# Kernel optimization log

Measured on AMD Instinct MI355X. Metric: run time of the kernel, lower is better.

The kernel has to match this reference:

```python
import jax, jax.numpy as jnp
import numpy as np

NUM_LABELS = 80
GROUPS = 512
OUT_PER_GROUP = 4  # 2048 / 512
K = 14  # kernel == spatial size -> 1x1 output


def setup_inputs() -> dict:
    key = jax.random.key(0)
    ks = jax.random.split(key, 8)
    B = 256
    x = jax.random.normal(ks[0], (B, NUM_LABELS, K, K), dtype=jnp.float32)
    # conv1: 1x1, num_labels -> 512 (store as [out,in])
    w1 = jax.random.normal(ks[1], (512, NUM_LABELS), dtype=jnp.float32) * 0.05
    b1 = jax.random.normal(ks[2], (512,), dtype=jnp.float32) * 0.01
    # conv2: 1x1, 512 -> 512
    w2 = jax.random.normal(ks[3], (512, 512), dtype=jnp.float32) * 0.05
    b2 = jax.random.normal(ks[4], (512,), dtype=jnp.float32) * 0.01
    # conv3 (grouped): per group, 1 in-ch -> 4 out-ch, 14x14 kernel, no bias
    w3 = jax.random.normal(ks[5], (GROUPS, OUT_PER_GROUP, K, K), dtype=jnp.float32) * 0.02
    # fc: 2048 -> num_labels (torch Linear layout [out,in])
    fc_w = jax.random.normal(ks[6], (NUM_LABELS, GROUPS * OUT_PER_GROUP), dtype=jnp.float32) * 0.02
    fc_b = jax.random.normal(ks[7], (NUM_LABELS,), dtype=jnp.float32) * 0.01
    return {"x": x, "w1": w1, "b1": b1, "w2": w2, "b2": b2,
            "w3": w3, "fc_w": fc_w, "fc_b": fc_b}


def reference(x, w1, b1, w2, b2, w3, fc_w, fc_b):
    # conv1: 1x1 conv == channel GEMM. x: [B,C,H,W]
    h = jnp.einsum('bchw,oc->bohw', x, w1) + b1[None, :, None, None]
    # conv2: 1x1 conv, 512 -> 512
    h = jnp.einsum('bchw,oc->bohw', h, w2) + b2[None, :, None, None]
    # conv3: 512 independent group convs (1 in-ch each, full 14x14 kernel,
    # no padding) -> output spatial 1x1. Fused into a single contraction.
    # h: [B, G, H, W], w3: [G, O, H, W] -> [B, G, O]
    g = jnp.einsum('bghw,gohw->bgo', h, w3)
    g = jax.nn.relu(g)
    # torch.cat over groups then flatten == reshape [B, G*O]
    flat = g.reshape(g.shape[0], GROUPS * OUT_PER_GROUP)
    return flat @ fc_w.T + fc_b
```

## Files before the change

### kernel.cpp

```cpp
#include <hip/hip_runtime.h>
#include <hip/hip_bf16.h>

#define CIN 80
#define NSP 196
#define HWP 208
#define KP  96
#define XST 104

#define NBA 4096
#define NBB 1024
#define NBC 512
#define NBD 64
#define NBE 16

typedef __attribute__((ext_vector_type(8))) short  short8;
typedef __attribute__((ext_vector_type(4))) float  floatx4;
typedef __attribute__((ext_vector_type(4))) unsigned short ushort4v;

static __device__ __forceinline__ unsigned short f2b(float f) {
    __hip_bfloat16 h = __float2bfloat16(f);
    return *(unsigned short*)&h;
}
static __device__ __forceinline__ float b2f(unsigned short u) {
    unsigned int x = ((unsigned int)u) << 16;
    float f; __builtin_memcpy(&f, &x, 4); return f;
}

__global__ __launch_bounds__(384) void kPre(
    const float* __restrict__ x,  const float* __restrict__ w1,
    const float* __restrict__ b1, const float* __restrict__ w2,
    const float* __restrict__ b2, const float* __restrict__ w3,
    const float* __restrict__ fc_w, const float* __restrict__ fc_b,
    float* __restrict__ Wcf, unsigned short* __restrict__ xbf,
    unsigned short* __restrict__ w3tb, unsigned short* __restrict__ fctb,
    float* __restrict__ out)
{
    __shared__ float tile[80 * 53];
    const int blk = blockIdx.x, t = threadIdx.x;

    if (blk < NBA) {
        const int o4 = blk >> 5, kc = blk & 31;
        const int lc = t % 96, oi = t / 96;
        const int o = o4 * 4 + oi;
        const int m0 = kc * 16;
        if (lc <= CIN) {
            const float* __restrict__ w2p = w2 + (size_t)o * 512 + m0;
            float part = 0.f;
            if (lc < CIN) {
                const float* __restrict__ w1p = w1 + (size_t)m0 * CIN + lc;
                #pragma unroll
                for (int i = 0; i < 16; ++i)
                    part = fmaf(w2p[i], w1p[(size_t)i * CIN], part);
            } else {
                #pragma unroll
                for (int i = 0; i < 16; ++i)
                    part = fmaf(w2p[i], b1[m0 + i], part);
                if (kc == 31) part += b2[o];
            }
            atomicAdd(Wcf + o * KP + lc, part);
        }
    } else if (blk < NBA + NBB) {
        const int r = blk - NBA;
        const int b = r >> 2, qt = r & 3, hw0 = qt * 52;
        for (int idx = t; idx < 80 * 52; idx += 384) {
            const int k = idx / 52, hl = idx - k * 52;
            const int hw = hw0 + hl;
            tile[k * 53 + hl] = (hw < NSP) ? x[(size_t)b * CIN * NSP + k * NSP + hw] : 0.f;
        }
        __syncthreads();
        unsigned short* __restrict__ ob = xbf + (size_t)b * HWP * KP;
        for (int idx = t; idx < 52 * 24; idx += 384) {
            const int hl = idx / 24, kq = idx - hl * 24;
            const int hw = hw0 + hl;
            ushort4v v;
            #pragma unroll
            for (int j = 0; j < 4; ++j) {
                const int k = kq * 4 + j;
                float f = 0.f;
                if (hw < NSP) {
                    if (k < CIN) f = tile[k * 53 + hl];
                    else if (k == CIN) f = 1.f;
                }
                v[j] = f2b(f);
            }
            *(ushort4v*)(ob + (size_t)hw * KP + kq * 4) = v;
        }
    } else if (blk < NBA + NBB + NBC) {
        const int g = blk - NBA - NBB;
        if (t < HWP) {
            ushort4v v;
            #pragma unroll
            for (int o = 0; o < 4; ++o)
                v[o] = f2b((t < NSP) ? w3[(size_t)g * 4 * NSP + o * NSP + t] : 0.f);
            *(ushort4v*)(w3tb + ((size_t)g * HWP + t) * 4) = v;
        }
    } else if (blk < NBA + NBB + NBC + NBD) {
        const int base = (blk - NBA - NBB - NBC) * 2560;
        for (int i = t; i < 2560; i += 384) {
            const int idx = base + i;
            const int k = idx / CIN, l = idx - k * CIN;
            fctb[idx] = f2b(fc_w[(size_t)l * 2048 + k]);
        }
    } else {
        const int base = (blk - NBA - NBB - NBC - NBD) * 1280;
        for (int i = t; i < 1280; i += 384) {
            const int idx = base + i;
            out[idx] = fc_b[idx - (idx / CIN) * CIN];
        }
    }
}

__global__ __launch_bounds__(512) void kM(
    const unsigned short* __restrict__ xbf, const float* __restrict__ Wcf,
    const unsigned short* __restrict__ w3tb, const unsigned short* __restrict__ fctb,
    float* __restrict__ out)
{
    __shared__ __align__(16) unsigned short xs[HWP * XST];
    __shared__ float gl[512];
    const int b = blockIdx.x, gc = blockIdx.y;
    const int t = threadIdx.x;

    {
        const ushort4v* __restrict__ src = (const ushort4v*)(xbf + (size_t)b * HWP * KP);
        for (int idx = t; idx < HWP * 24; idx += 512) {
            const int r = idx / 24, c = idx - r * 24;
            *(ushort4v*)(xs + r * XST + c * 4) = src[r * 24 + c];
        }
    }

    const int w = t >> 6, lane = t & 63;
    const int col = lane & 15, quad = lane >> 4;
    const int g0 = gc * 128 + w * 16;

    short8 A[3];
    {
        const float* __restrict__ ap = Wcf + (size_t)(g0 + col) * KP + quad * 8;
        #pragma unroll
        for (int ks = 0; ks < 3; ++ks) {
            const floatx4 lo = *(const floatx4*)(ap + ks * 32);
            const floatx4 hi = *(const floatx4*)(ap + ks * 32 + 4);
            short8 s;
            #pragma unroll
            for (int j = 0; j < 4; ++j) {
                s[j]     = (short)f2b(lo[j]);
                s[4 + j] = (short)f2b(hi[j]);
            }
            A[ks] = s;
        }
    }

    float p[4][4];
    #pragma unroll
    for (int r = 0; r < 4; ++r)
        #pragma unroll
        for (int o = 0; o < 4; ++o) p[r][o] = 0.f;

    const unsigned short* __restrict__ wb =
        w3tb + ((size_t)(g0 + quad * 4) * HWP + col) * 4;
    const unsigned short* __restrict__ xrow = xs + col * XST + quad * 8;

    __syncthreads();

    ushort4v cw[4];
    #pragma unroll
    for (int r = 0; r < 4; ++r)
        cw[r] = *(const ushort4v*)(wb + (size_t)r * HWP * 4);

    #pragma unroll 1
    for (int nt = 0; nt < 13; ++nt) {
        const int ntn = (nt < 12) ? nt + 1 : 12;
        ushort4v nw[4];
        #pragma unroll
        for (int r = 0; r < 4; ++r)
            nw[r] = *(const ushort4v*)(wb + ((size_t)r * HWP + ntn * 16) * 4);

        const unsigned short* __restrict__ xp = xrow + nt * 16 * XST;
        const short8 x0 = *(const short8*)(xp);
        const short8 x1 = *(const short8*)(xp + 32);
        const short8 x2 = *(const short8*)(xp + 64);
        floatx4 acc = {0.f, 0.f, 0.f, 0.f};
        acc = __builtin_amdgcn_mfma_f32_16x16x32_bf16(A[0], x0, acc, 0, 0, 0);
        acc = __builtin_amdgcn_mfma_f32_16x16x32_bf16(A[1], x1, acc, 0, 0, 0);
        acc = __builtin_amdgcn_mfma_f32_16x16x32_bf16(A[2], x2, acc, 0, 0, 0);

        #pragma unroll
        for (int r = 0; r < 4; ++r) {
            p[r][0] = fmaf(acc[r], b2f(cw[r][0]), p[r][0]);
            p[r][1] = fmaf(acc[r], b2f(cw[r][1]), p[r][1]);
            p[r][2] = fmaf(acc[r], b2f(cw[r][2]), p[r][2]);
            p[r][3] = fmaf(acc[r], b2f(cw[r][3]), p[r][3]);
        }
        #pragma unroll
        for (int r = 0; r < 4; ++r) cw[r] = nw[r];
    }

    #pragma unroll
    for (int r = 0; r < 4; ++r) {
        float q0 = p[r][0], q1 = p[r][1], q2 = p[r][2], q3 = p[r][3];
        #pragma unroll
        for (int s = 8; s >= 1; s >>= 1) {
            q0 += __shfl_down(q0, s, 16);
            q1 += __shfl_down(q1, s, 16);
            q2 += __shfl_down(q2, s, 16);
            q3 += __shfl_down(q3, s, 16);
        }
        if (col == 0) {
            const int glocal = w * 16 + quad * 4 + r;
            floatx4 ov = {fmaxf(q0, 0.f), fmaxf(q1, 0.f), fmaxf(q2, 0.f), fmaxf(q3, 0.f)};
            *(floatx4*)(gl + glocal * 4) = ov;
        }
    }
    __syncthreads();

    if (t < 320) {
        const int l = t % CIN, q = t / CIN;
        const unsigned short* __restrict__ fr =
            fctb + (size_t)(gc * 512 + q * 128) * CIN + l;
        const float* __restrict__ gp = gl + q * 128;
        float s = 0.f;
        #pragma unroll 4
        for (int kk = 0; kk < 128; ++kk)
            s = fmaf(gp[kk], b2f(fr[(size_t)kk * CIN]), s);
        atomicAdd(out + b * CIN + l, s);
    }
}

extern "C" void kernel_launch(void* const* d_in, const int* in_sizes, int n_in,
                              void* d_out, int out_size, void* d_ws, size_t ws_size,
                              hipStream_t stream) {
    const float* x    = (const float*)d_in[0];
    const float* w1   = (const float*)d_in[1];
    const float* b1   = (const float*)d_in[2];
    const float* w2   = (const float*)d_in[3];
    const float* b2   = (const float*)d_in[4];
    const float* w3   = (const float*)d_in[5];
    const float* fc_w = (const float*)d_in[6];
    const float* fc_b = (const float*)d_in[7];
    float* out = (float*)d_out;

    const int B = in_sizes[0] / (CIN * NSP);

    char* ws = (char*)d_ws;
    unsigned short* xbf = (unsigned short*)ws;
    size_t off = (size_t)B * HWP * KP * 2;
    float* Wcf = (float*)(ws + off);                   off += 512 * KP * 4;
    unsigned short* w3tb = (unsigned short*)(ws + off); off += (size_t)512 * HWP * 4 * 2;
    unsigned short* fctb = (unsigned short*)(ws + off);

    hipMemsetAsync(Wcf, 0, 512 * KP * 4, stream);
    kPre<<<NBA + NBB + NBC + NBD + NBE, 384, 0, stream>>>(
        x, w1, b1, w2, b2, w3, fc_w, fc_b, Wcf, xbf, w3tb, fctb, out);
    kM<<<dim3(B, 4), 512, 0, stream>>>(xbf, Wcf, w3tb, fctb, out);
}
```

Baseline: 139.4 us.

## Process two M-tiles per warp and halve grid to reuse staged x tile

Each block now covers 256 groups instead of 128, with each warp computing two 16-row MFMA tiles that share the same x fragments from shared memory. The grid drops from B×4 to B×2 blocks, halving the per-block global-to-LDS staging of the input slab and the number of fc atomics. The software prefetch of w3 weights for the next iteration is removed; weights are loaded inside the loop. This costs more registers per thread and leaves fewer blocks to hide latency.

```diff
diff --git a/kernel.cpp b/kernel.cpp
--- a/kernel.cpp
+++ b/kernel.cpp
@@ -116,7 +116,7 @@
     float* __restrict__ out)
 {
     __shared__ __align__(16) unsigned short xs[HWP * XST];
-    __shared__ float gl[512];
+    __shared__ float gl[1024];
     const int b = blockIdx.x, gc = blockIdx.y;
     const int t = threadIdx.x;
 
@@ -124,17 +124,18 @@
         const ushort4v* __restrict__ src = (const ushort4v*)(xbf + (size_t)b * HWP * KP);
         for (int idx = t; idx < HWP * 24; idx += 512) {
             const int r = idx / 24, c = idx - r * 24;
-            *(ushort4v*)(xs + r * XST + c * 4) = src[r * 24 + c];
+            *(ushort4v*)(xs + r * XST + c * 4) = src[idx];
         }
     }
 
     const int w = t >> 6, lane = t & 63;
     const int col = lane & 15, quad = lane >> 4;
-    const int g0 = gc * 128 + w * 16;
-
-    short8 A[3];
-    {
-        const float* __restrict__ ap = Wcf + (size_t)(g0 + col) * KP + quad * 8;
+    const int gb = gc * 256 + w * 32;
+
+    short8 A[2][3];
+    #pragma unroll
+    for (int mt = 0; mt < 2; ++mt) {
+        const float* __restrict__ ap = Wcf + (size_t)(gb + mt * 16 + col) * KP + quad * 8;
         #pragma unroll
         for (int ks = 0; ks < 3; ++ks) {
             const floatx4 lo = *(const floatx4*)(ap + ks * 32);
@@ -145,81 +146,86 @@
                 s[j]     = (short)f2b(lo[j]);
                 s[4 + j] = (short)f2b(hi[j]);
             }
-            A[ks] = s;
-        }
-    }
-
-    float p[4][4];
+            A[mt][ks] = s;
+        }
+    }
+
+    float p[2][4][4];
     #pragma unroll
-    for (int r = 0; r < 4; ++r)
-        #pragma unroll
-        for (int o = 0; o < 4; ++o) p[r][o] = 0.f;
-
-    const unsigned short* __restrict__ wb =
-        w3tb + ((size_t)(g0 + quad * 4) * HWP + col) * 4;
+    for (int mt = 0; mt < 2; ++mt)
+        #pragma unroll
+        for (int r = 0; r < 4; ++r)
+            #pragma unroll
+            for (int o = 0; o < 4; ++o) p[mt][r][o] = 0.f;
+
     const unsigned short* __restrict__ xrow = xs + col * XST + quad * 8;
+    const unsigned short* __restrict__ wb0 =
+        w3tb + ((size_t)(gb + quad * 4) * HWP + col) * 4;
+    const unsigned short* __restrict__ wb1 =
+        w3tb + ((size_t)(gb + 16 + quad * 4) * HWP + col) * 4;
 
     __syncthreads();
-
-    ushort4v cw[4];
-    #pragma unroll
-    for (int r = 0; r < 4; ++r)
-        cw[r] = *(const ushort4v*)(wb + (size_t)r * HWP * 4);
 
     #pragma unroll 1
     for (int nt = 0; nt < 13; ++nt) {
-        const int ntn = (nt < 12) ? nt + 1 : 12;
-        ushort4v nw[4];
-        #pragma unroll
-        for (int r = 0; r < 4; ++r)
-            nw[r] = *(const ushort4v*)(wb + ((size_t)r * HWP + ntn * 16) * 4);
-
+        ushort4v wv0[4], wv1[4];
+        #pragma unroll
+        for (int r = 0; r < 4; ++r) {
+            wv0[r] = *(const ushort4v*)(wb0 + ((size_t)r * HWP + nt * 16) * 4);
+            wv1[r] = *(const ushort4v*)(wb1 + ((size_t)r * HWP + nt * 16) * 4);
+        }
         const unsigned short* __restrict__ xp = xrow + nt * 16 * XST;
         const short8 x0 = *(const short8*)(xp);
         const short8 x1 = *(const short8*)(xp + 32);
         const short8 x2 = *(const short8*)(xp + 64);
-        floatx4 acc = {0.f, 0.f, 0.f, 0.f};
-        acc = __builtin_amdgcn_mfma_f32_16x16x32_bf16(A[0], x0, acc, 0, 0, 0);
-        acc = __builtin_amdgcn_mfma_f32_16x16x32_bf16(A[1], x1, acc, 0, 0, 0);
-        acc = __builtin_amdgcn_mfma_f32_16x16x32_bf16(A[2], x2, acc, 0, 0, 0);
-
+        floatx4 a0 = {0.f, 0.f, 0.f, 0.f}, a1 = {0.f, 0.f, 0.f, 0.f};
+        a0 = __builtin_amdgcn_mfma_f32_16x16x32_bf16(A[0][0], x0, a0, 0, 0, 0);
+        a0 = __builtin_amdgcn_mfma_f32_16x16x32_bf16(A[0][1], x1, a0, 0, 0, 0);
+        a0 = __builtin_amdgcn_mfma_f32_16x16x32_bf16(A[0][2], x2, a0, 0, 0, 0);
+        a1 = __builtin_amdgcn_mfma_f32_16x16x32_bf16(A[1][0], x0, a1, 0, 0, 0);
+        a1 = __builtin_amdgcn_mfma_f32_16x16x32_bf16(A[1][1], x1, a1, 0, 0, 0);
+        a1 = __builtin_amdgcn_mfma_f32_16x16x32_bf16(A[1][2], x2, a1, 0, 0, 0);
         #pragma unroll
         for (int r = 0; r < 4; ++r) {
-            p[r][0] = fmaf(acc[r], b2f(cw[r][0]), p[r][0]);
-            p[r][1] = fmaf(acc[r], b2f(cw[r][1]), p[r][1]);
-            p[r][2] = fmaf(acc[r], b2f(cw[r][2]), p[r][2]);
-            p[r][3] = fmaf(acc[r], b2f(cw[r][3]), p[r][3]);
-        }
-        #pragma unroll
-        for (int r = 0; r < 4; ++r) cw[r] = nw[r];
+            p[0][r][0] = fmaf(a0[r], b2f(wv0[r][0]), p[0][r][0]);
+            p[0][r][1] = fmaf(a0[r], b2f(wv0[r][1]), p[0][r][1]);
+            p[0][r][2] = fmaf(a0[r], b2f(wv0[r][2]), p[0][r][2]);
+            p[0][r][3] = fmaf(a0[r], b2f(wv0[r][3]), p[0][r][3]);
+            p[1][r][0] = fmaf(a1[r], b2f(wv1[r][0]), p[1][r][0]);
+            p[1][r][1] = fmaf(a1[r], b2f(wv1[r][1]), p[1][r][1]);
+            p[1][r][2] = fmaf(a1[r], b2f(wv1[r][2]), p[1][r][2]);
+            p[1][r][3] = fmaf(a1[r], b2f(wv1[r][3]), p[1][r][3]);
+        }
     }
 
     #pragma unroll
-    for (int r = 0; r < 4; ++r) {
-        float q0 = p[r][0], q1 = p[r][1], q2 = p[r][2], q3 = p[r][3];
-        #pragma unroll
-        for (int s = 8; s >= 1; s >>= 1) {
-            q0 += __shfl_down(q0, s, 16);
-            q1 += __shfl_down(q1, s, 16);
-            q2 += __shfl_down(q2, s, 16);
-            q3 += __shfl_down(q3, s, 16);
-        }
-        if (col == 0) {
-            const int glocal = w * 16 + quad * 4 + r;
-            floatx4 ov = {fmaxf(q0, 0.f), fmaxf(q1, 0.f), fmaxf(q2, 0.f), fmaxf(q3, 0.f)};
-            *(floatx4*)(gl + glocal * 4) = ov;
-        }
-    }
+    for (int mt = 0; mt < 2; ++mt)
+        #pragma unroll
+        for (int r = 0; r < 4; ++r) {
+            float q0 = p[mt][r][0], q1 = p[mt][r][1], q2 = p[mt][r][2], q3 = p[mt][r][3];
+            #pragma unroll
+            for (int s = 8; s >= 1; s >>= 1) {
+                q0 += __shfl_down(q0, s, 16);
+                q1 += __shfl_down(q1, s, 16);
+                q2 += __shfl_down(q2, s, 16);
+                q3 += __shfl_down(q3, s, 16);
+            }
+            if (col == 0) {
+                const int glocal = w * 32 + mt * 16 + quad * 4 + r;
+                floatx4 ov = {fmaxf(q0, 0.f), fmaxf(q1, 0.f), fmaxf(q2, 0.f), fmaxf(q3, 0.f)};
+                *(floatx4*)(gl + glocal * 4) = ov;
+            }
+        }
     __syncthreads();
 
     if (t < 320) {
         const int l = t % CIN, q = t / CIN;
         const unsigned short* __restrict__ fr =
-            fctb + (size_t)(gc * 512 + q * 128) * CIN + l;
-        const float* __restrict__ gp = gl + q * 128;
+            fctb + (size_t)(gc * 1024 + q * 256) * CIN + l;
+        const float* __restrict__ gp = gl + q * 256;
         float s = 0.f;
         #pragma unroll 4
-        for (int kk = 0; kk < 128; ++kk)
+        for (int kk = 0; kk < 256; ++kk)
             s = fmaf(gp[kk], b2f(fr[(size_t)kk * CIN]), s);
         atomicAdd(out + b * CIN + l, s);
     }
@@ -250,5 +256,5 @@
     hipMemsetAsync(Wcf, 0, 512 * KP * 4, stream);
     kPre<<<NBA + NBB + NBC + NBD + NBE, 384, 0, stream>>>(
         x, w1, b1, w2, b2, w3, fc_w, fc_b, Wcf, xbf, w3tb, fctb, out);
-    kM<<<dim3(B, 4), 512, 0, stream>>>(xbf, Wcf, w3tb, fctb, out);
-}
+    kM<<<dim3(B, 2), 512, 0, stream>>>(xbf, Wcf, w3tb, fctb, out);
+}
```

Result: no change. 138.3 us (-0.8%).
